# Optimization experiments

Hardware: AMD Instinct MI355X
Metric: run time of the kernel (lower is better)

## Reference

```python
import jax, jax.numpy as jnp
import numpy as np

B = 4
MAX_N = 2048
D = 512
H = 8
HD = D // H
SRC_LENS = [2048, 1536, 1800, 1200]   # sum = 6584
REF_LENS = [1900, 2048, 1400, 1600]   # sum = 6948
NEG_INF = -1e9


def setup_inputs() -> dict:
    key = jax.random.key(0)
    ks = jax.random.split(key, 8)
    n_src, n_ref = sum(SRC_LENS), sum(REF_LENS)
    s = 0.02
    return {
        "feats_src": jax.random.normal(ks[0], (n_src, D), dtype=jnp.float32),
        "batch_src": jnp.asarray(np.repeat(np.arange(B), SRC_LENS), dtype=jnp.int32),
        "feats_ref": jax.random.normal(ks[1], (n_ref, D), dtype=jnp.float32),
        "batch_ref": jnp.asarray(np.repeat(np.arange(B), REF_LENS), dtype=jnp.int32),
        "w_in": jax.random.normal(ks[2], (3 * D, D), dtype=jnp.float32) * s,
        "b_in": jnp.zeros((3 * D,), dtype=jnp.float32),
        "w_out": jax.random.normal(ks[3], (D, D), dtype=jnp.float32) * s,
        "b_out": jnp.zeros((D,), dtype=jnp.float32),
        "gw1": jax.random.normal(ks[4], (D, D), dtype=jnp.float32) * s,
        "gb1": jnp.zeros((D,), dtype=jnp.float32),
        "gw2": jax.random.normal(ks[5], (1, D), dtype=jnp.float32) * s,
        "gb2": jnp.zeros((1,), dtype=jnp.float32),
    }


def _to_dense(feats, batch_idx):
    # sparse [N, D] (sorted batch indices) -> dense [B, MAX_N, D] + key_padding_mask
    n = feats.shape[0]
    counts = jax.ops.segment_sum(jnp.ones((n,), jnp.int32), batch_idx, num_segments=B)
    starts = jnp.concatenate([jnp.zeros((1,), jnp.int32), jnp.cumsum(counts)[:-1].astype(jnp.int32)])
    pos = jnp.arange(n, dtype=jnp.int32) - starts[batch_idx]  # position within batch
    dense = jnp.zeros((B, MAX_N, feats.shape[1]), feats.dtype).at[batch_idx, pos].set(feats)
    mask = jnp.arange(MAX_N)[None, :] >= counts[:, None]  # True = padding (key_padding_mask)
    return dense, mask, pos


def reference(feats_src, batch_src, feats_ref, batch_ref,
              w_in, b_in, w_out, b_out, gw1, gb1, gw2, gb2):
    d_src, mask_src, pos_src = _to_dense(feats_src, batch_src)
    d_ref, mask_ref, _ = _to_dense(feats_ref, batch_ref)

    # nn.MultiheadAttention (batch_first, eval mode): packed in_proj, scaled dot-product
    q = (d_src @ w_in[:D].T + b_in[:D]).reshape(B, MAX_N, H, HD)
    k = (d_ref @ w_in[D:2 * D].T + b_in[D:2 * D]).reshape(B, MAX_N, H, HD)
    v = (d_ref @ w_in[2 * D:].T + b_in[2 * D:]).reshape(B, MAX_N, H, HD)
    scores = jnp.einsum('bqhd,bkhd->bhqk', q * (HD ** -0.5), k)
    scores = jnp.where(mask_ref[:, None, None, :], NEG_INF, scores)
    attn = jax.nn.softmax(scores, axis=-1)
    ctx = jnp.einsum('bhqk,bkhd->bqhd', attn, v).reshape(B, MAX_N, D)
    d_aligned = ctx @ w_out.T + b_out

    # gate MLP: Linear -> ReLU -> Linear -> Sigmoid
    gate = jax.nn.sigmoid(jax.nn.relu(d_aligned @ gw1.T + gb1) @ gw2.T + gb2)  # [B, MAX_N, 1]
    d_out = d_src + gate * d_aligned

    # dense -> ragged: gather each token back to its flat slot
    out_flat = d_out[batch_src, pos_src]  # [N_src, D]
    return out_flat, gate
```

## Files before the change

### kernel.cpp

```cpp
#include <hip/hip_runtime.h>
#include <hip/hip_bf16.h>


typedef __bf16 bf16x8_t __attribute__((ext_vector_type(8)));
typedef __bf16 bf16x4_t __attribute__((ext_vector_type(4)));
typedef float f32x4_t __attribute__((ext_vector_type(4)));
typedef float f32x2_t __attribute__((ext_vector_type(2)));

__device__ inline bf16x8_t zero8() {
  bf16x8_t z;
#pragma unroll
  for (int t = 0; t < 8; ++t) z[t] = (__bf16)0.0f;
  return z;
}

__device__ __forceinline__ int sniff_f32(const void* w) {
  unsigned short u = ((const unsigned short*)w)[threadIdx.x & 63];
  return __ballot((u & 0x7F80) >= 0x3F80) != 0ULL;
}

__global__ void sentinel_k(float* out) {
  if (threadIdx.x == 0 && blockIdx.x == 0) out[0] = 1000.0f;
}

__global__ void cv_all(const void* w_in, const void* b_in, const void* w_out,
                       const void* b_out, const void* gw1, const void* gb1,
                       const void* gw2, const void* gb2,
                       __hip_bfloat16* __restrict__ ws) {
  int f = sniff_f32(w_in);
  const size_t F_W_IN = 16, F_B_IN = 786448, F_W_OUT = 787984, F_B_OUT = 1050128,
               F_GW1 = 1050640, F_GB1 = 1312784, F_GW2 = 1313296, F_GB2 = 1313808;
  const int total = 1313793;
  for (int g = blockIdx.x * 256 + threadIdx.x; g < total; g += gridDim.x * 256) {
    const void* src;
    size_t dst;
    int i;
    if (g < 786432) { src = w_in; dst = F_W_IN; i = g; }
    else if (g < 787968) { src = b_in; dst = F_B_IN; i = g - 786432; }
    else if (g < 1050112) { src = w_out; dst = F_W_OUT; i = g - 787968; }
    else if (g < 1050624) { src = b_out; dst = F_B_OUT; i = g - 1050112; }
    else if (g < 1312768) { src = gw1; dst = F_GW1; i = g - 1050624; }
    else if (g < 1313280) { src = gb1; dst = F_GB1; i = g - 1312768; }
    else if (g < 1313792) { src = gw2; dst = F_GW2; i = g - 1313280; }
    else { src = gb2; dst = F_GB2; i = g - 1313792; }
    ws[dst + i] = f ? __float2bfloat16(((const float*)src)[i])
                    : ((const __hip_bfloat16*)src)[i];
  }
}

template <bool AF32>
__global__ __launch_bounds__(256) void gemm128(
    const void* __restrict__ A_, long aoff, const __hip_bfloat16* __restrict__ Bt,
    const __hip_bfloat16* __restrict__ bias, __hip_bfloat16* __restrict__ C,
    int M, int K, int lda, int ldb, int ldc, float cscale, int relu,
    const void* snf) {
  __shared__ __bf16 As[128][64];
  __shared__ __bf16 Bs[128][64];
  int f = 0;
  if constexpr (AF32) f = sniff_f32(snf);
  int tid = threadIdx.x, lane = tid & 63, wave = tid >> 6;
  int wm = wave >> 1, wn = wave & 1;
  int l15 = lane & 15, quad = lane >> 4;
  int bm = blockIdx.x * 128, bn = blockIdx.y * 128;

  f32x4_t acc[4][4];
#pragma unroll
  for (int i = 0; i < 4; ++i)
#pragma unroll
    for (int j = 0; j < 4; ++j)
#pragma unroll
      for (int r = 0; r < 4; ++r) acc[i][j][r] = 0.f;

  bf16x8_t ra[4], rb[4];
  f32x4_t raf[4][2];

  auto gload = [&](int k0) {
#pragma unroll
    for (int s = 0; s < 4; ++s) {
      int id = s * 256 + tid;
      int row = id >> 3, col = (id & 7) * 8;
      int arow = bm + row;
      if (AF32 && f) {
        if (arow < M) {
          const float* p = (const float*)A_ + aoff + (size_t)arow * lda + k0 + col;
          raf[s][0] = *reinterpret_cast<const f32x4_t*>(p);
          raf[s][1] = *reinterpret_cast<const f32x4_t*>(p + 4);
        } else {
#pragma unroll
          for (int e = 0; e < 4; ++e) { raf[s][0][e] = 0.f; raf[s][1][e] = 0.f; }
        }
      } else {
        ra[s] = (arow < M)
                    ? *reinterpret_cast<const bf16x8_t*>((const __hip_bfloat16*)A_ + aoff +
                                                         (size_t)arow * lda + k0 + col)
                    : zero8();
      }
      rb[s] = *reinterpret_cast<const bf16x8_t*>(Bt + (size_t)(bn + row) * ldb + k0 + col);
    }
  };
  auto stage = [&]() {
#pragma unroll
    for (int s = 0; s < 4; ++s) {
      int id = s * 256 + tid;
      int row = id >> 3, col = (id & 7) * 8;
      if (AF32 && f) {
        bf16x8_t t;
#pragma unroll
        for (int e = 0; e < 4; ++e) {
          t[e] = (__bf16)raf[s][0][e];
          t[4 + e] = (__bf16)raf[s][1][e];
        }
        *reinterpret_cast<bf16x8_t*>(&As[row][col]) = t;
      } else {
        *reinterpret_cast<bf16x8_t*>(&As[row][col]) = ra[s];
      }
      *reinterpret_cast<bf16x8_t*>(&Bs[row][col]) = rb[s];
    }
  };

  int nk = K >> 6;
  gload(0);
  for (int it = 0; it < nk; ++it) {
    stage();
    __syncthreads();
    if (it + 1 < nk) gload((it + 1) * 64);
#pragma unroll
    for (int ks = 0; ks < 2; ++ks) {
      bf16x8_t af[4], bfv[4];
#pragma unroll
      for (int i = 0; i < 4; ++i)
        af[i] = *reinterpret_cast<const bf16x8_t*>(
            &As[wm * 64 + i * 16 + l15][ks * 32 + quad * 8]);
#pragma unroll
      for (int j = 0; j < 4; ++j)
        bfv[j] = *reinterpret_cast<const bf16x8_t*>(
            &Bs[wn * 64 + j * 16 + l15][ks * 32 + quad * 8]);
#pragma unroll
      for (int i = 0; i < 4; ++i)
#pragma unroll
        for (int j = 0; j < 4; ++j)
          acc[i][j] = __builtin_amdgcn_mfma_f32_16x16x32_bf16(af[i], bfv[j], acc[i][j], 0, 0, 0);
    }
    __syncthreads();
  }

#pragma unroll
  for (int i = 0; i < 4; ++i)
#pragma unroll
    for (int j = 0; j < 4; ++j) {
      int col = bn + wn * 64 + j * 16 + l15;
      float bv = __bfloat162float(bias[col]);
#pragma unroll
      for (int r = 0; r < 4; ++r) {
        int row = bm + wm * 64 + i * 16 + quad * 4 + r;
        if (row < M) {
          float v = (acc[i][j][r] + bv) * cscale;
          if (relu) v = fmaxf(v, 0.f);
          C[(size_t)row * ldc + col] = __float2bfloat16(v);
        }
      }
    }
}

__global__ __launch_bounds__(256) void gemm128_pv(
    const __hip_bfloat16* __restrict__ P0, const __hip_bfloat16* __restrict__ P1,
    const float* __restrict__ L, const __hip_bfloat16* __restrict__ Bt,
    const __hip_bfloat16* __restrict__ bias, __hip_bfloat16* __restrict__ C,
    int M) {
  __shared__ __bf16 As[128][64];
  __shared__ __bf16 Bs[128][64];
  int tid = threadIdx.x, lane = tid & 63, wave = tid >> 6;
  int wm = wave >> 1, wn = wave & 1;
  int l15 = lane & 15, quad = lane >> 4;
  int bm = blockIdx.x * 128, bn = blockIdx.y * 128;

  f32x4_t acc[4][4];
#pragma unroll
  for (int i = 0; i < 4; ++i)
#pragma unroll
    for (int j = 0; j < 4; ++j)
#pragma unroll
      for (int r = 0; r < 4; ++r) acc[i][j][r] = 0.f;

  bf16x8_t rp0[4], rp1[4], rb[4];
  f32x2_t rl[4];

  auto gload = [&](int k0) {
    int h = k0 >> 6;
#pragma unroll
    for (int s = 0; s < 4; ++s) {
      int id = s * 256 + tid;
      int row = id >> 3, col = (id & 7) * 8;
      int arow = bm + row;
      if (arow < M) {
        size_t off = (size_t)arow * 512 + k0 + col;
        rp0[s] = *reinterpret_cast<const bf16x8_t*>(P0 + off);
        rp1[s] = *reinterpret_cast<const bf16x8_t*>(P1 + off);
        rl[s] = *reinterpret_cast<const f32x2_t*>(&L[((size_t)arow * 8 + h) * 2]);
      } else {
        rp0[s] = zero8();
        rp1[s] = zero8();
        rl[s][0] = 1.f;
        rl[s][1] = 0.f;
      }
      rb[s] = *reinterpret_cast<const bf16x8_t*>(Bt + (size_t)(bn + row) * 512 + k0 + col);
    }
  };
  auto stage = [&]() {
#pragma unroll
    for (int s = 0; s < 4; ++s) {
      int id = s * 256 + tid;
      int row = id >> 3, col = (id & 7) * 8;
      float sc = 1.0f / (rl[s][0] + rl[s][1]);
      float w0 = rl[s][0] * sc, w1 = rl[s][1] * sc;
      bf16x8_t t;
#pragma unroll
      for (int e = 0; e < 8; ++e)
        t[e] = (__bf16)(w0 * (float)rp0[s][e] + w1 * (float)rp1[s][e]);
      *reinterpret_cast<bf16x8_t*>(&As[row][col]) = t;
      *reinterpret_cast<bf16x8_t*>(&Bs[row][col]) = rb[s];
    }
  };

  gload(0);
  for (int it = 0; it < 8; ++it) {
    stage();
    __syncthreads();
    if (it + 1 < 8) gload((it + 1) * 64);
#pragma unroll
    for (int ks = 0; ks < 2; ++ks) {
      bf16x8_t af[4], bfv[4];
#pragma unroll
      for (int i = 0; i < 4; ++i)
        af[i] = *reinterpret_cast<const bf16x8_t*>(
            &As[wm * 64 + i * 16 + l15][ks * 32 + quad * 8]);
#pragma unroll
      for (int j = 0; j < 4; ++j)
        bfv[j] = *reinterpret_cast<const bf16x8_t*>(
            &Bs[wn * 64 + j * 16 + l15][ks * 32 + quad * 8]);
#pragma unroll
      for (int i = 0; i < 4; ++i)
#pragma unroll
        for (int j = 0; j < 4; ++j)
          acc[i][j] = __builtin_amdgcn_mfma_f32_16x16x32_bf16(af[i], bfv[j], acc[i][j], 0, 0, 0);
    }
    __syncthreads();
  }

#pragma unroll
  for (int i = 0; i < 4; ++i)
#pragma unroll
    for (int j = 0; j < 4; ++j) {
      int col = bn + wn * 64 + j * 16 + l15;
      float bv = __bfloat162float(bias[col]);
#pragma unroll
      for (int r = 0; r < 4; ++r) {
        int row = bm + wm * 64 + i * 16 + quad * 4 + r;
        if (row < M)
          C[(size_t)row * 512 + col] = __float2bfloat16(acc[i][j][r] + bv);
      }
    }
}

__device__ __forceinline__ void flash_core(
    const __hip_bfloat16* __restrict__ Qb, const __hip_bfloat16* __restrict__ KVb,
    __hip_bfloat16* __restrict__ OUTb, float* __restrict__ LPb, int nsrc, int nref,
    int qt, int kt0, int ktNfull, int do_tail,
    __bf16 (&VtL)[2][64][72], __bf16 (&PL)[4][32][72]) {
  int h = blockIdx.y;
  int tid = threadIdx.x, lane = tid & 63, wave = tid >> 6;
  int l15 = lane & 15, quad = lane >> 4;
  int Mb = nsrc + 1;
  int qbase = qt * 128 + wave * 32;

  bf16x8_t qfr[2][2];
#pragma unroll
  for (int g = 0; g < 2; ++g) {
    int qrow = qbase + g * 16 + l15;
#pragma unroll
    for (int ks = 0; ks < 2; ++ks)
      qfr[g][ks] = (qrow < nsrc)
                       ? *reinterpret_cast<const bf16x8_t*>(
                             Qb + (size_t)qrow * 512 + h * 64 + ks * 32 + quad * 8)
                       : zero8();
  }

  f32x4_t O[2][4];
#pragma unroll
  for (int g = 0; g < 2; ++g)
#pragma unroll
    for (int j = 0; j < 4; ++j)
#pragma unroll
      for (int r = 0; r < 4; ++r) O[g][j][r] = 0.f;
  float lsum[2] = {0.f, 0.f};

  bf16x8_t kf[8], v0, v1;
  auto loadK = [&](int k0) {
#pragma unroll
    for (int j = 0; j < 4; ++j) {
      const __hip_bfloat16* kp =
          KVb + (size_t)(k0 + j * 16 + l15) * 1024 + h * 64 + quad * 8;
      kf[j * 2] = *reinterpret_cast<const bf16x8_t*>(kp);
      kf[j * 2 + 1] = *reinterpret_cast<const bf16x8_t*>(kp + 32);
    }
  };
  auto loadV = [&](int k0) {
    const __hip_bfloat16* vp = KVb + (size_t)(k0 + lane) * 1024 + 512 + h * 64 + wave * 16;
    v0 = *reinterpret_cast<const bf16x8_t*>(vp);
    v1 = *reinterpret_cast<const bf16x8_t*>(vp + 8);
  };

  int nit = ktNfull - kt0;
  if (nit > 0) {
    loadK(kt0 * 64);
    loadV(kt0 * 64);
  }

  for (int it = 0; it < nit; ++it) {
    int k0 = (kt0 + it) * 64;
    __bf16(*Vt)[72] = VtL[it & 1];
#pragma unroll
    for (int e = 0; e < 8; ++e) {
      Vt[wave * 16 + e][lane] = v0[e];
      Vt[wave * 16 + 8 + e][lane] = v1[e];
    }
    if (it + 1 < nit) loadV(k0 + 64);

    f32x4_t St[2][4];
#pragma unroll
    for (int g = 0; g < 2; ++g)
#pragma unroll
      for (int j = 0; j < 4; ++j)
#pragma unroll
        for (int r = 0; r < 4; ++r) St[g][j][r] = 0.f;
#pragma unroll
    for (int g = 0; g < 2; ++g)
#pragma unroll
      for (int j = 0; j < 4; ++j)
#pragma unroll
        for (int ks = 0; ks < 2; ++ks)
          St[g][j] = __builtin_amdgcn_mfma_f32_16x16x32_bf16(kf[j * 2 + ks], qfr[g][ks],
                                                             St[g][j], 0, 0, 0);
    if (it + 1 < nit) loadK(k0 + 64);

#pragma unroll
    for (int g = 0; g < 2; ++g)
#pragma unroll
      for (int j = 0; j < 4; ++j) {
        bf16x4_t pk;
#pragma unroll
        for (int r = 0; r < 4; ++r) {
          float p = exp2f(St[g][j][r]);
          lsum[g] += p;
          pk[r] = (__bf16)p;
        }
        *reinterpret_cast<bf16x4_t*>(&PL[wave][g * 16 + l15][j * 16 + quad * 4]) = pk;
      }

    __syncthreads();

    bf16x8_t pa[2][2];
#pragma unroll
    for (int g = 0; g < 2; ++g)
#pragma unroll
      for (int ks = 0; ks < 2; ++ks)
        pa[g][ks] = *reinterpret_cast<const bf16x8_t*>(
            &PL[wave][g * 16 + l15][ks * 32 + quad * 8]);
#pragma unroll
    for (int j = 0; j < 4; ++j)
#pragma unroll
      for (int ks = 0; ks < 2; ++ks) {
        bf16x8_t vb =
            *reinterpret_cast<const bf16x8_t*>(&Vt[j * 16 + l15][ks * 32 + quad * 8]);
#pragma unroll
        for (int g = 0; g < 2; ++g)
          O[g][j] = __builtin_amdgcn_mfma_f32_16x16x32_bf16(pa[g][ks], vb, O[g][j], 0, 0, 0);
      }
  }

  if (do_tail) {
    int k0 = ktNfull * 64;
    __bf16(*Vt)[72] = VtL[nit & 1];
    {
      int kr = k0 + lane;
      const __hip_bfloat16* vp = KVb + (size_t)kr * 1024 + 512 + h * 64 + wave * 16;
      bf16x8_t t0 = (kr < nref) ? *reinterpret_cast<const bf16x8_t*>(vp) : zero8();
      bf16x8_t t1 = (kr < nref) ? *reinterpret_cast<const bf16x8_t*>(vp + 8) : zero8();
#pragma unroll
      for (int e = 0; e < 8; ++e) {
        Vt[wave * 16 + e][lane] = t0[e];
        Vt[wave * 16 + 8 + e][lane] = t1[e];
      }
    }
#pragma unroll
    for (int j = 0; j < 4; ++j) {
      int kcol = k0 + j * 16 + l15;
      const __hip_bfloat16* kp = KVb + (size_t)kcol * 1024 + h * 64 + quad * 8;
      kf[j * 2] = (kcol < nref) ? *reinterpret_cast<const bf16x8_t*>(kp) : zero8();
      kf[j * 2 + 1] = (kcol < nref) ? *reinterpret_cast<const bf16x8_t*>(kp + 32) : zero8();
    }
#pragma unroll
    for (int g = 0; g < 2; ++g) {
      f32x4_t St[4];
#pragma unroll
      for (int j = 0; j < 4; ++j)
#pragma unroll
        for (int r = 0; r < 4; ++r) St[j][r] = 0.f;
#pragma unroll
      for (int j = 0; j < 4; ++j)
#pragma unroll
        for (int ks = 0; ks < 2; ++ks)
          St[j] = __builtin_amdgcn_mfma_f32_16x16x32_bf16(kf[j * 2 + ks], qfr[g][ks],
                                                          St[j], 0, 0, 0);
#pragma unroll
      for (int j = 0; j < 4; ++j) {
        bf16x4_t pk;
#pragma unroll
        for (int r = 0; r < 4; ++r) {
          int kl = k0 + j * 16 + quad * 4 + r;
          float p = (kl < nref) ? exp2f(St[j][r]) : 0.f;
          lsum[g] += p;
          pk[r] = (__bf16)p;
        }
        *reinterpret_cast<bf16x4_t*>(&PL[wave][g * 16 + l15][j * 16 + quad * 4]) = pk;
      }
    }
    __syncthreads();
    bf16x8_t pa[2][2];
#pragma unroll
    for (int g = 0; g < 2; ++g)
#pragma unroll
      for (int ks = 0; ks < 2; ++ks)
        pa[g][ks] = *reinterpret_cast<const bf16x8_t*>(
            &PL[wave][g * 16 + l15][ks * 32 + quad * 8]);
#pragma unroll
    for (int j = 0; j < 4; ++j)
#pragma unroll
      for (int ks = 0; ks < 2; ++ks) {
        bf16x8_t vb =
            *reinterpret_cast<const bf16x8_t*>(&Vt[j * 16 + l15][ks * 32 + quad * 8]);
#pragma unroll
        for (int g = 0; g < 2; ++g)
          O[g][j] = __builtin_amdgcn_mfma_f32_16x16x32_bf16(pa[g][ks], vb, O[g][j], 0, 0, 0);
      }
  }

#pragma unroll
  for (int g = 0; g < 2; ++g) {
    lsum[g] += __shfl_xor(lsum[g], 16);
    lsum[g] += __shfl_xor(lsum[g], 32);
  }

  if (LPb && quad == 0) {
#pragma unroll
    for (int g = 0; g < 2; ++g) {
      int row = qbase + g * 16 + l15;
      if (row < Mb) LPb[((size_t)row * 8 + h) * 2] = lsum[g];
    }
  }

#pragma unroll
  for (int g = 0; g < 2; ++g)
#pragma unroll
    for (int r = 0; r < 4; ++r) {
      int row = qbase + g * 16 + quad * 4 + r;
      if (row < Mb) {
        float li = __shfl(lsum[g], quad * 4 + r);
        float inv = 1.0f / li;
#pragma unroll
        for (int j = 0; j < 4; ++j)
          OUTb[(size_t)row * 512 + h * 64 + j * 16 + l15] =
              __float2bfloat16(O[g][j][r] * inv);
      }
    }
}

__global__ __launch_bounds__(256) void flash_all(
    const __hip_bfloat16* __restrict__ Q, const __hip_bfloat16* __restrict__ KV,
    __hip_bfloat16* __restrict__ O0, __hip_bfloat16* __restrict__ O1,
    float* __restrict__ L, int nsplit) {
  const int TILE_START[4] = {0, 17, 30, 45};
  const int SRC_START[4] = {0, 2048, 3584, 5384};
  const int REF_START[4] = {0, 1900, 3948, 5348};
  const int SRC_LEN[4] = {2048, 1536, 1800, 1200};
  const int REF_LEN[4] = {1900, 2048, 1400, 1600};
  const int CS[4] = {0, 2049, 3586, 5387};
  __shared__ __bf16 VtL[2][64][72];
  __shared__ __bf16 PL[4][32][72];
  int bid = blockIdx.x;
  int b = (bid >= TILE_START[3]) ? 3 : (bid >= TILE_START[2]) ? 2 : (bid >= TILE_START[1]) ? 1 : 0;
  int qt = bid - TILE_START[b];
  int nref = REF_LEN[b];
  int full = nref >> 6, nkt = (nref + 63) >> 6, rem = nref & 63;
  int split = blockIdx.z;
  int kt0, ktN, tail;
  if (nsplit == 1) { kt0 = 0; ktN = full; tail = rem > 0; }
  else if (split == 0) { int half = nkt >> 1; kt0 = 0; ktN = half; tail = 0; }
  else { int half = nkt >> 1; kt0 = half; ktN = full; tail = rem > 0; }
  __hip_bfloat16* OUT = (nsplit == 1 || split == 0) ? O0 : O1;
  float* LP = (nsplit == 1) ? nullptr : (L + split + (size_t)CS[b] * 16);
  flash_core(Q + (size_t)SRC_START[b] * 512, KV + (size_t)REF_START[b] * 1024,
             OUT + (size_t)CS[b] * 512, LP, SRC_LEN[b], nref, qt, kt0, ktN, tail, VtL, PL);
}

__global__ __launch_bounds__(256) void flash_one(const __hip_bfloat16* __restrict__ Qb,
                                                 const __hip_bfloat16* __restrict__ KVb,
                                                 __hip_bfloat16* __restrict__ OUTb,
                                                 int nsrc, int nref) {
  __shared__ __bf16 VtL[2][64][72];
  __shared__ __bf16 PL[4][32][72];
  flash_core(Qb, KVb, OUTb, nullptr, nsrc, nref, blockIdx.x, 0, nref >> 6,
             (nref & 63) > 0, VtL, PL);
}

__global__ __launch_bounds__(256) void finalize_all(
    const void* __restrict__ src, const __hip_bfloat16* __restrict__ aligned,
    const __hip_bfloat16* __restrict__ hidden, const __hip_bfloat16* __restrict__ gw2,
    const __hip_bfloat16* __restrict__ gb2, void* __restrict__ out, const void* snf) {
  int f = sniff_f32(snf);
  int lane = threadIdx.x & 63;
  int r = blockIdx.x * 4 + (threadIdx.x >> 6);
  int b = (r >= 5387) ? 3 : (r >= 3586) ? 2 : (r >= 2049) ? 1 : 0;
  const int CS[4] = {0, 2049, 3586, 5387};
  const int NSRC[4] = {2048, 1536, 1800, 1200};
  int pos = r - CS[b];

  float zacc = 0.f;
  const __hip_bfloat16* hrow = hidden + (size_t)r * 512;
#pragma unroll
  for (int t = 0; t < 8; ++t) {
    int c = lane + (t << 6);
    zacc += __bfloat162float(hrow[c]) * __bfloat162float(gw2[c]);
  }
  for (int o = 32; o; o >>= 1) zacc += __shfl_xor(zacc, o);
  zacc += __bfloat162float(gb2[0]);
  float g = 1.f / (1.f + __expf(-zacc));

  const size_t GOFF = (size_t)6584 * 512;
  if (pos < NSRC[b]) {
    size_t ib = (size_t)(r - b) * 512;
    const __hip_bfloat16* arow = aligned + (size_t)r * 512;
#pragma unroll
    for (int t = 0; t < 8; ++t) {
      int c = lane + (t << 6);
      float sv = f ? ((const float*)src)[ib + c]
                   : __bfloat162float(((const __hip_bfloat16*)src)[ib + c]);
      float val = sv + g * __bfloat162float(arow[c]);
      if (f) ((float*)out)[ib + c] = val;
      else ((__hip_bfloat16*)out)[ib + c] = __float2bfloat16(val);
    }
    if (lane == 0) {
      size_t go = GOFF + b * 2048 + pos;
      if (f) ((float*)out)[go] = g;
      else ((__hip_bfloat16*)out)[go] = __float2bfloat16(g);
    }
  } else {
    for (int p = NSRC[b] + lane; p < 2048; p += 64) {
      size_t go = GOFF + b * 2048 + p;
      if (f) ((float*)out)[go] = g;
      else ((__hip_bfloat16*)out)[go] = __float2bfloat16(g);
    }
  }
}

__global__ __launch_bounds__(256) void finalize_b(
    const void* __restrict__ src, const __hip_bfloat16* __restrict__ alnb,
    const __hip_bfloat16* __restrict__ hidb, const __hip_bfloat16* __restrict__ gw2,
    const __hip_bfloat16* __restrict__ gb2, void* __restrict__ out,
    int b, int nsrc, int src_start, const void* snf) {
  int f = sniff_f32(snf);
  int lane = threadIdx.x & 63;
  int r = blockIdx.x * 4 + (threadIdx.x >> 6);
  if (r > nsrc) return;

  float zacc = 0.f;
  const __hip_bfloat16* hrow = hidb + (size_t)r * 512;
#pragma unroll
  for (int t = 0; t < 8; ++t) {
    int c = lane + (t << 6);
    zacc += __bfloat162float(hrow[c]) * __bfloat162float(gw2[c]);
  }
  for (int o = 32; o; o >>= 1) zacc += __shfl_xor(zacc, o);
  zacc += __bfloat162float(gb2[0]);
  float g = 1.f / (1.f + __expf(-zacc));

  const size_t GOFF = (size_t)6584 * 512;
  if (r < nsrc) {
    size_t ib = (size_t)(src_start + r) * 512;
    const __hip_bfloat16* arow = alnb + (size_t)r * 512;
#pragma unroll
    for (int t = 0; t < 8; ++t) {
      int c = lane + (t << 6);
      float sv = f ? ((const float*)src)[ib + c]
                   : __bfloat162float(((const __hip_bfloat16*)src)[ib + c]);
      float val = sv + g * __bfloat162float(arow[c]);
      if (f) ((float*)out)[ib + c] = val;
      else ((__hip_bfloat16*)out)[ib + c] = __float2bfloat16(val);
    }
    if (lane == 0) {
      size_t go = GOFF + b * 2048 + r;
      if (f) ((float*)out)[go] = g;
      else ((__hip_bfloat16*)out)[go] = __float2bfloat16(g);
    }
  } else {
    for (int p = nsrc + lane; p < 2048; p += 64) {
      size_t go = GOFF + b * 2048 + p;
      if (f) ((float*)out)[go] = g;
      else ((__hip_bfloat16*)out)[go] = __float2bfloat16(g);
    }
  }
}

extern "C" void kernel_launch(void* const* d_in, const int* in_sizes, int n_in,
                              void* d_out, int out_size, void* d_ws, size_t ws_size,
                              hipStream_t stream) {
  (void)in_sizes; (void)n_in; (void)out_size;
  const void* feats_src = d_in[0];
  const void* feats_ref = d_in[2];
  const void* w_in = d_in[4];
  const void* b_in = d_in[5];
  const void* w_out = d_in[6];
  const void* b_out = d_in[7];
  const void* gw1 = d_in[8];
  const void* gb1 = d_in[9];
  const void* gw2 = d_in[10];
  const void* gb2 = d_in[11];

  const size_t F_W_IN = 16, F_B_IN = 786448, F_W_OUT = 787984, F_B_OUT = 1050128,
               F_GW1 = 1050640, F_GB1 = 1312784, F_GW2 = 1313296, F_GB2 = 1313808,
               A0 = 1313824;
  const size_t NEED_A2 = 2 * 22139936;
  const size_t NEED_A = 2 * 15178784;
  const size_t NEED_B = 2 * (A0 + 4259840);
  const float CQ = 0.18033688011112042f;

  if (ws_size < NEED_B) {
    sentinel_k<<<1, 64, 0, stream>>>((float*)d_out);
    return;
  }

  __hip_bfloat16* ws = (__hip_bfloat16*)d_ws;
  cv_all<<<dim3(1024), dim3(256), 0, stream>>>(w_in, b_in, w_out, b_out, gw1, gb1, gw2,
                                               gb2, ws);

  const int SRC_LEN[4] = {2048, 1536, 1800, 1200};
  const int REF_LEN[4] = {1900, 2048, 1400, 1600};
  const int SRC_START[4] = {0, 2048, 3584, 5384};
  const int REF_START[4] = {0, 1900, 3948, 5348};
  dim3 blk(256);

  if (ws_size >= NEED_A) {
    __hip_bfloat16* R1 = ws + A0;
    __hip_bfloat16* R2 = R1 + 3375104;
    __hip_bfloat16* R3 = R2 + 7114752;
    gemm128<true><<<dim3(52, 4), blk, 0, stream>>>(feats_src, 0, ws + F_W_IN,
                                                   ws + F_B_IN, R1, 6584, 512, 512, 512,
                                                   512, CQ, 0, w_in);
    gemm128<true><<<dim3(55, 8), blk, 0, stream>>>(feats_ref, 0, ws + F_W_IN + 262144,
                                                   ws + F_B_IN + 512, R2, 6948, 512, 512,
                                                   512, 1024, 1.0f, 0, w_in);
    if (ws_size >= NEED_A2) {
      __hip_bfloat16* P0 = R3 + 3375104;
      __hip_bfloat16* P1 = P0 + 3375104;
      float* L = (float*)(ws + 21928992);
      flash_all<<<dim3(55, 8, 2), blk, 0, stream>>>(R1, R2, P0, P1, L, 2);
      gemm128_pv<<<dim3(52, 4), blk, 0, stream>>>(P0, P1, L, ws + F_W_OUT, ws + F_B_OUT,
                                                  R1, 6588);
    } else {
      flash_all<<<dim3(55, 8, 1), blk, 0, stream>>>(R1, R2, R3, nullptr, nullptr, 1);
      gemm128<false><<<dim3(52, 4), blk, 0, stream>>>(R3, 0, ws + F_W_OUT, ws + F_B_OUT,
                                                      R1, 6588, 512, 512, 512, 512, 1.0f,
                                                      0, nullptr);
    }
    gemm128<false><<<dim3(52, 4), blk, 0, stream>>>(R1, 0, ws + F_GW1, ws + F_GB1, R3,
                                                    6588, 512, 512, 512, 512, 1.0f, 1,
                                                    nullptr);
    finalize_all<<<dim3(1647), blk, 0, stream>>>(feats_src, R1, R3, ws + F_GW2,
                                                 ws + F_GB2, d_out, w_in);
  } else {
    __hip_bfloat16* W2 = ws + A0;
    __hip_bfloat16* W1 = W2 + 2097152;
    __hip_bfloat16* W3 = W1 + 1081344;
    for (int b = 0; b < 4; ++b) {
      int nsrc = SRC_LEN[b], nref = REF_LEN[b];
      gemm128<true><<<dim3((nsrc + 127) / 128, 4), blk, 0, stream>>>(
          feats_src, (long)SRC_START[b] * 512, ws + F_W_IN, ws + F_B_IN, W1, nsrc, 512,
          512, 512, 512, CQ, 0, w_in);
      gemm128<true><<<dim3((nref + 127) / 128, 8), blk, 0, stream>>>(
          feats_ref, (long)REF_START[b] * 512, ws + F_W_IN + 262144, ws + F_B_IN + 512,
          W2, nref, 512, 512, 512, 1024, 1.0f, 0, w_in);
      flash_one<<<dim3((nsrc + 128) / 128, 8), blk, 0, stream>>>(W1, W2, W3, nsrc, nref);
      gemm128<false><<<dim3((nsrc + 128) / 128, 4), blk, 0, stream>>>(
          W3, 0, ws + F_W_OUT, ws + F_B_OUT, W1, nsrc + 1, 512, 512, 512, 512, 1.0f, 0,
          nullptr);
      gemm128<false><<<dim3((nsrc + 128) / 128, 4), blk, 0, stream>>>(
          W1, 0, ws + F_GW1, ws + F_GB1, W3, nsrc + 1, 512, 512, 512, 512, 1.0f, 1,
          nullptr);
      finalize_b<<<dim3((nsrc + 4) / 4), blk, 0, stream>>>(
          feats_src, W1, W3, ws + F_GW2, ws + F_GB2, d_out, b, nsrc, SRC_START[b], w_in);
    }
  }
}
```

Before: 261.4 us.

## Fuse QKV projections, fold weight conversion into flash, fuse gate MLP with finalize

Merges the Q and KV projection GEMMs into one launch that reads fp32 inputs and weights directly, converting them while staging into shared memory. This drops the w_in conversion pass. The remaining weight conversion moves into extra blocks of the flash attention grid, so it overlaps with attention work. The gate MLP (GEMM, ReLU, dot with gw2, sigmoid) is fused with the residual finalize, so the hidden activation is never written out. In exchange, the fused gate kernel runs on only 103 blocks and recomputes its B tiles, which may underuse the GPU.

```diff
diff --git a/kernel.cpp b/kernel.cpp
--- a/kernel.cpp
+++ b/kernel.cpp
@@ -6,6 +6,8 @@
 typedef __bf16 bf16x4_t __attribute__((ext_vector_type(4)));
 typedef float f32x4_t __attribute__((ext_vector_type(4)));
 typedef float f32x2_t __attribute__((ext_vector_type(2)));
+
+#define CQ_SCALE 0.18033688011112042f
 
 __device__ inline bf16x8_t zero8() {
   bf16x8_t z;
@@ -48,6 +50,138 @@
   }
 }
 
+__device__ __forceinline__ void proj_core(
+    const void* __restrict__ A_, const void* __restrict__ B_,
+    const void* __restrict__ bias_, long biasoff, __hip_bfloat16* __restrict__ C,
+    int M, int ldc, float cscale, int f, int brow0, int bm, int bn,
+    __bf16 (&As)[128][64], __bf16 (&Bs)[128][64]) {
+  int tid = threadIdx.x, lane = tid & 63, wave = tid >> 6;
+  int wm = wave >> 1, wn = wave & 1;
+  int l15 = lane & 15, quad = lane >> 4;
+
+  f32x4_t acc[4][4];
+#pragma unroll
+  for (int i = 0; i < 4; ++i)
+#pragma unroll
+    for (int j = 0; j < 4; ++j)
+#pragma unroll
+      for (int r = 0; r < 4; ++r) acc[i][j][r] = 0.f;
+
+  bf16x8_t ra[4], rb[4];
+  f32x4_t raf[4][2], rbf[4][2];
+
+  auto gload = [&](int k0) {
+#pragma unroll
+    for (int s = 0; s < 4; ++s) {
+      int id = s * 256 + tid;
+      int row = id >> 3, col = (id & 7) * 8;
+      int arow = bm + row;
+      size_t boffe = (size_t)(brow0 + bn + row) * 512 + k0 + col;
+      if (f) {
+        if (arow < M) {
+          const float* p = (const float*)A_ + (size_t)arow * 512 + k0 + col;
+          raf[s][0] = *reinterpret_cast<const f32x4_t*>(p);
+          raf[s][1] = *reinterpret_cast<const f32x4_t*>(p + 4);
+        } else {
+#pragma unroll
+          for (int e = 0; e < 4; ++e) { raf[s][0][e] = 0.f; raf[s][1][e] = 0.f; }
+        }
+        const float* q = (const float*)B_ + boffe;
+        rbf[s][0] = *reinterpret_cast<const f32x4_t*>(q);
+        rbf[s][1] = *reinterpret_cast<const f32x4_t*>(q + 4);
+      } else {
+        ra[s] = (arow < M)
+                    ? *reinterpret_cast<const bf16x8_t*>((const __hip_bfloat16*)A_ +
+                                                         (size_t)arow * 512 + k0 + col)
+                    : zero8();
+        rb[s] = *reinterpret_cast<const bf16x8_t*>((const __hip_bfloat16*)B_ + boffe);
+      }
+    }
+  };
+  auto stage = [&]() {
+#pragma unroll
+    for (int s = 0; s < 4; ++s) {
+      int id = s * 256 + tid;
+      int row = id >> 3, col = (id & 7) * 8;
+      if (f) {
+        bf16x8_t ta, tb;
+#pragma unroll
+        for (int e = 0; e < 4; ++e) {
+          ta[e] = (__bf16)raf[s][0][e];
+          ta[4 + e] = (__bf16)raf[s][1][e];
+          tb[e] = (__bf16)rbf[s][0][e];
+          tb[4 + e] = (__bf16)rbf[s][1][e];
+        }
+        *reinterpret_cast<bf16x8_t*>(&As[row][col]) = ta;
+        *reinterpret_cast<bf16x8_t*>(&Bs[row][col]) = tb;
+      } else {
+        *reinterpret_cast<bf16x8_t*>(&As[row][col]) = ra[s];
+        *reinterpret_cast<bf16x8_t*>(&Bs[row][col]) = rb[s];
+      }
+    }
+  };
+
+  gload(0);
+  for (int it = 0; it < 8; ++it) {
+    stage();
+    __syncthreads();
+    if (it + 1 < 8) gload((it + 1) * 64);
+#pragma unroll
+    for (int ks = 0; ks < 2; ++ks) {
+      bf16x8_t af[4], bfv[4];
+#pragma unroll
+      for (int i = 0; i < 4; ++i)
+        af[i] = *reinterpret_cast<const bf16x8_t*>(
+            &As[wm * 64 + i * 16 + l15][ks * 32 + quad * 8]);
+#pragma unroll
+      for (int j = 0; j < 4; ++j)
+        bfv[j] = *reinterpret_cast<const bf16x8_t*>(
+            &Bs[wn * 64 + j * 16 + l15][ks * 32 + quad * 8]);
+#pragma unroll
+      for (int i = 0; i < 4; ++i)
+#pragma unroll
+        for (int j = 0; j < 4; ++j)
+          acc[i][j] = __builtin_amdgcn_mfma_f32_16x16x32_bf16(af[i], bfv[j], acc[i][j], 0, 0, 0);
+    }
+    __syncthreads();
+  }
+
+#pragma unroll
+  for (int i = 0; i < 4; ++i)
+#pragma unroll
+    for (int j = 0; j < 4; ++j) {
+      int col = bn + wn * 64 + j * 16 + l15;
+      float bv = f ? ((const float*)bias_)[biasoff + col]
+                   : __bfloat162float(((const __hip_bfloat16*)bias_)[biasoff + col]);
+#pragma unroll
+      for (int r = 0; r < 4; ++r) {
+        int row = bm + wm * 64 + i * 16 + quad * 4 + r;
+        if (row < M)
+          C[(size_t)row * ldc + col] = __float2bfloat16((acc[i][j][r] + bv) * cscale);
+      }
+    }
+}
+
+__global__ __launch_bounds__(256) void proj_all(
+    const void* __restrict__ fs, const void* __restrict__ fr,
+    const void* __restrict__ w_in_, const void* __restrict__ b_in_,
+    __hip_bfloat16* __restrict__ Q, __hip_bfloat16* __restrict__ KV) {
+  __shared__ __bf16 As[128][64];
+  __shared__ __bf16 Bs[128][64];
+  int f = sniff_f32(w_in_);
+  int bid = blockIdx.x;
+  if (bid < 208) {
+    int bx = bid >> 2, by = bid & 3;
+    proj_core(fs, w_in_, b_in_, 0, Q, 6584, 512, CQ_SCALE, f, 0, bx * 128, by * 128,
+              As, Bs);
+  } else {
+    int k = bid - 208;
+    int bx = k >> 3, by = k & 7;
+    proj_core(fr, w_in_, b_in_, 512, KV, 6948, 1024, 1.0f, f, 512, bx * 128, by * 128,
+              As, Bs);
+  }
+}
+
 template <bool AF32>
 __global__ __launch_bounds__(256) void gemm128(
     const void* __restrict__ A_, long aoff, const __hip_bfloat16* __restrict__ Bt,
@@ -370,11 +504,11 @@
     for (int j = 0; j < 4; ++j)
 #pragma unroll
       for (int ks = 0; ks < 2; ++ks) {
-        bf16x8_t vb =
+        bf16x8_t vbf =
             *reinterpret_cast<const bf16x8_t*>(&Vt[j * 16 + l15][ks * 32 + quad * 8]);
 #pragma unroll
         for (int g = 0; g < 2; ++g)
-          O[g][j] = __builtin_amdgcn_mfma_f32_16x16x32_bf16(pa[g][ks], vb, O[g][j], 0, 0, 0);
+          O[g][j] = __builtin_amdgcn_mfma_f32_16x16x32_bf16(pa[g][ks], vbf, O[g][j], 0, 0, 0);
       }
   }
 
@@ -437,11 +571,11 @@
     for (int j = 0; j < 4; ++j)
 #pragma unroll
       for (int ks = 0; ks < 2; ++ks) {
-        bf16x8_t vb =
+        bf16x8_t vbf =
             *reinterpret_cast<const bf16x8_t*>(&Vt[j * 16 + l15][ks * 32 + quad * 8]);
 #pragma unroll
         for (int g = 0; g < 2; ++g)
-          O[g][j] = __builtin_amdgcn_mfma_f32_16x16x32_bf16(pa[g][ks], vb, O[g][j], 0, 0, 0);
+          O[g][j] = __builtin_amdgcn_mfma_f32_16x16x32_bf16(pa[g][ks], vbf, O[g][j], 0, 0, 0);
       }
   }
 
@@ -478,15 +612,38 @@
 __global__ __launch_bounds__(256) void flash_all(
     const __hip_bfloat16* __restrict__ Q, const __hip_bfloat16* __restrict__ KV,
     __hip_bfloat16* __restrict__ O0, __hip_bfloat16* __restrict__ O1,
-    float* __restrict__ L, int nsplit) {
+    float* __restrict__ L, int nsplit, const void* w_out, const void* b_out,
+    const void* gw1, const void* gb1, const void* gw2, const void* gb2,
+    __hip_bfloat16* __restrict__ ws, const void* snf) {
+  __shared__ __bf16 VtL[2][64][72];
+  __shared__ __bf16 PL[4][32][72];
+  if (blockIdx.x >= 55) {
+    int f = sniff_f32(snf);
+    int nconv = 2 * gridDim.y * gridDim.z;
+    int cid = ((blockIdx.x - 55) * gridDim.y + blockIdx.y) * gridDim.z + blockIdx.z;
+    const size_t F_W_OUT = 787984, F_B_OUT = 1050128, F_GW1 = 1050640,
+                 F_GB1 = 1312784, F_GW2 = 1313296, F_GB2 = 1313808;
+    for (int g = cid * 256 + threadIdx.x; g < 525825; g += nconv * 256) {
+      const void* src;
+      size_t dst;
+      int i;
+      if (g < 262144) { src = w_out; dst = F_W_OUT; i = g; }
+      else if (g < 262656) { src = b_out; dst = F_B_OUT; i = g - 262144; }
+      else if (g < 524800) { src = gw1; dst = F_GW1; i = g - 262656; }
+      else if (g < 525312) { src = gb1; dst = F_GB1; i = g - 524800; }
+      else if (g < 525824) { src = gw2; dst = F_GW2; i = g - 525312; }
+      else { src = gb2; dst = F_GB2; i = g - 525824; }
+      ws[dst + i] = f ? __float2bfloat16(((const float*)src)[i])
+                      : ((const __hip_bfloat16*)src)[i];
+    }
+    return;
+  }
   const int TILE_START[4] = {0, 17, 30, 45};
   const int SRC_START[4] = {0, 2048, 3584, 5384};
   const int REF_START[4] = {0, 1900, 3948, 5348};
   const int SRC_LEN[4] = {2048, 1536, 1800, 1200};
   const int REF_LEN[4] = {1900, 2048, 1400, 1600};
   const int CS[4] = {0, 2049, 3586, 5387};
-  __shared__ __bf16 VtL[2][64][72];
-  __shared__ __bf16 PL[4][32][72];
   int bid = blockIdx.x;
   int b = (bid >= TILE_START[3]) ? 3 : (bid >= TILE_START[2]) ? 2 : (bid >= TILE_START[1]) ? 1 : 0;
   int qt = bid - TILE_START[b];
@@ -513,52 +670,133 @@
              (nref & 63) > 0, VtL, PL);
 }
 
-__global__ __launch_bounds__(256) void finalize_all(
-    const void* __restrict__ src, const __hip_bfloat16* __restrict__ aligned,
-    const __hip_bfloat16* __restrict__ hidden, const __hip_bfloat16* __restrict__ gw2,
-    const __hip_bfloat16* __restrict__ gb2, void* __restrict__ out, const void* snf) {
-  int f = sniff_f32(snf);
-  int lane = threadIdx.x & 63;
-  int r = blockIdx.x * 4 + (threadIdx.x >> 6);
-  int b = (r >= 5387) ? 3 : (r >= 3586) ? 2 : (r >= 2049) ? 1 : 0;
+__global__ __launch_bounds__(256) void gate_fin(
+    const void* __restrict__ src, const __hip_bfloat16* __restrict__ ALN,
+    const __hip_bfloat16* __restrict__ gw1b, const __hip_bfloat16* __restrict__ gb1b,
+    const __hip_bfloat16* __restrict__ gw2b, const __hip_bfloat16* __restrict__ gb2b,
+    void* __restrict__ out, const void* snf) {
+  __shared__ __bf16 As[64][64];
+  __shared__ __bf16 Bs[128][64];
   const int CS[4] = {0, 2049, 3586, 5387};
   const int NSRC[4] = {2048, 1536, 1800, 1200};
-  int pos = r - CS[b];
-
-  float zacc = 0.f;
-  const __hip_bfloat16* hrow = hidden + (size_t)r * 512;
-#pragma unroll
-  for (int t = 0; t < 8; ++t) {
-    int c = lane + (t << 6);
-    zacc += __bfloat162float(hrow[c]) * __bfloat162float(gw2[c]);
-  }
-  for (int o = 32; o; o >>= 1) zacc += __shfl_xor(zacc, o);
-  zacc += __bfloat162float(gb2[0]);
-  float g = 1.f / (1.f + __expf(-zacc));
+  int f = sniff_f32(snf);
+  int tid = threadIdx.x, lane = tid & 63, w = tid >> 6;
+  int l15 = lane & 15, quad = lane >> 4;
+  int bm = blockIdx.x * 64;
+
+  float gacc[4] = {0.f, 0.f, 0.f, 0.f};
+  bf16x8_t ra[2], rb[4];
+
+  for (int ct = 0; ct < 4; ++ct) {
+    int bnn = ct * 128;
+    f32x4_t acc[8];
+#pragma unroll
+    for (int j = 0; j < 8; ++j)
+#pragma unroll
+      for (int r = 0; r < 4; ++r) acc[j][r] = 0.f;
+
+    auto gload = [&](int k0) {
+#pragma unroll
+      for (int s = 0; s < 2; ++s) {
+        int id = s * 256 + tid;
+        int row = id >> 3, col = (id & 7) * 8;
+        int arow = bm + row;
+        ra[s] = (arow < 6588)
+                    ? *reinterpret_cast<const bf16x8_t*>(ALN + (size_t)arow * 512 + k0 + col)
+                    : zero8();
+      }
+#pragma unroll
+      for (int s = 0; s < 4; ++s) {
+        int id = s * 256 + tid;
+        int row = id >> 3, col = (id & 7) * 8;
+        rb[s] = *reinterpret_cast<const bf16x8_t*>(gw1b + (size_t)(bnn + row) * 512 + k0 + col);
+      }
+    };
+    auto stage = [&]() {
+#pragma unroll
+      for (int s = 0; s < 2; ++s) {
+        int id = s * 256 + tid;
+        *reinterpret_cast<bf16x8_t*>(&As[id >> 3][(id & 7) * 8]) = ra[s];
+      }
+#pragma unroll
+      for (int s = 0; s < 4; ++s) {
+        int id = s * 256 + tid;
+        *reinterpret_cast<bf16x8_t*>(&Bs[id >> 3][(id & 7) * 8]) = rb[s];
+      }
+    };
+
+    gload(0);
+    for (int it = 0; it < 8; ++it) {
+      stage();
+      __syncthreads();
+      if (it + 1 < 8) gload((it + 1) * 64);
+#pragma unroll
+      for (int ks = 0; ks < 2; ++ks) {
+        bf16x8_t af = *reinterpret_cast<const bf16x8_t*>(
+            &As[w * 16 + l15][ks * 32 + quad * 8]);
+#pragma unroll
+        for (int j = 0; j < 8; ++j) {
+          bf16x8_t bv = *reinterpret_cast<const bf16x8_t*>(
+              &Bs[j * 16 + l15][ks * 32 + quad * 8]);
+          acc[j] = __builtin_amdgcn_mfma_f32_16x16x32_bf16(af, bv, acc[j], 0, 0, 0);
+        }
+      }
+      __syncthreads();
+    }
+
+#pragma unroll
+    for (int j = 0; j < 8; ++j) {
+      int col = bnn + j * 16 + l15;
+      float b1 = __bfloat162float(gb1b[col]);
+      float w2 = __bfloat162float(gw2b[col]);
+#pragma unroll
+      for (int r = 0; r < 4; ++r) gacc[r] += fmaxf(acc[j][r] + b1, 0.f) * w2;
+    }
+  }
+
+#pragma unroll
+  for (int r = 0; r < 4; ++r) {
+    gacc[r] += __shfl_xor(gacc[r], 1);
+    gacc[r] += __shfl_xor(gacc[r], 2);
+    gacc[r] += __shfl_xor(gacc[r], 4);
+    gacc[r] += __shfl_xor(gacc[r], 8);
+  }
+  float gb2v = __bfloat162float(gb2b[0]);
+  float gv[4];
+#pragma unroll
+  for (int r = 0; r < 4; ++r) gv[r] = 1.f / (1.f + __expf(-(gacc[r] + gb2v)));
 
   const size_t GOFF = (size_t)6584 * 512;
-  if (pos < NSRC[b]) {
-    size_t ib = (size_t)(r - b) * 512;
-    const __hip_bfloat16* arow = aligned + (size_t)r * 512;
-#pragma unroll
-    for (int t = 0; t < 8; ++t) {
-      int c = lane + (t << 6);
-      float sv = f ? ((const float*)src)[ib + c]
-                   : __bfloat162float(((const __hip_bfloat16*)src)[ib + c]);
-      float val = sv + g * __bfloat162float(arow[c]);
-      if (f) ((float*)out)[ib + c] = val;
-      else ((__hip_bfloat16*)out)[ib + c] = __float2bfloat16(val);
-    }
-    if (lane == 0) {
-      size_t go = GOFF + b * 2048 + pos;
-      if (f) ((float*)out)[go] = g;
-      else ((__hip_bfloat16*)out)[go] = __float2bfloat16(g);
-    }
-  } else {
-    for (int p = NSRC[b] + lane; p < 2048; p += 64) {
-      size_t go = GOFF + b * 2048 + p;
-      if (f) ((float*)out)[go] = g;
-      else ((__hip_bfloat16*)out)[go] = __float2bfloat16(g);
+#pragma unroll
+  for (int rr = 0; rr < 16; ++rr) {
+    int row = bm + w * 16 + rr;
+    if (row >= 6588) continue;
+    float g = __shfl(gv[rr & 3], (rr >> 2) * 16);
+    int b = (row >= 5387) ? 3 : (row >= 3586) ? 2 : (row >= 2049) ? 1 : 0;
+    int pos = row - CS[b];
+    if (pos < NSRC[b]) {
+      size_t ib = (size_t)(row - b) * 512;
+      const __hip_bfloat16* arow = ALN + (size_t)row * 512;
+#pragma unroll
+      for (int t = 0; t < 8; ++t) {
+        int c = lane + (t << 6);
+        float sv = f ? ((const float*)src)[ib + c]
+                     : __bfloat162float(((const __hip_bfloat16*)src)[ib + c]);
+        float val = sv + g * __bfloat162float(arow[c]);
+        if (f) ((float*)out)[ib + c] = val;
+        else ((__hip_bfloat16*)out)[ib + c] = __float2bfloat16(val);
+      }
+      if (lane == 0) {
+        size_t go = GOFF + b * 2048 + pos;
+        if (f) ((float*)out)[go] = g;
+        else ((__hip_bfloat16*)out)[go] = __float2bfloat16(g);
+      }
+    } else {
+      for (int p = NSRC[b] + lane; p < 2048; p += 64) {
+        size_t go = GOFF + b * 2048 + p;
+        if (f) ((float*)out)[go] = g;
+        else ((__hip_bfloat16*)out)[go] = __float2bfloat16(g);
+      }
     }
   }
 }
@@ -632,7 +870,6 @@
   const size_t NEED_A2 = 2 * 22139936;
   const size_t NEED_A = 2 * 15178784;
   const size_t NEED_B = 2 * (A0 + 4259840);
-  const float CQ = 0.18033688011112042f;
 
   if (ws_size < NEED_B) {
     sentinel_k<<<1, 64, 0, stream>>>((float*)d_out);
@@ -640,9 +877,6 @@
   }
 
   __hip_bfloat16* ws = (__hip_bfloat16*)d_ws;
-  cv_all<<<dim3(1024), dim3(256), 0, stream>>>(w_in, b_in, w_out, b_out, gw1, gb1, gw2,
-                                               gb2, ws);
-
   const int SRC_LEN[4] = {2048, 1536, 1800, 1200};
   const int REF_LEN[4] = {1900, 2048, 1400, 1600};
   const int SRC_START[4] = {0, 2048, 3584, 5384};
@@ -653,31 +887,28 @@
     __hip_bfloat16* R1 = ws + A0;
     __hip_bfloat16* R2 = R1 + 3375104;
     __hip_bfloat16* R3 = R2 + 7114752;
-    gemm128<true><<<dim3(52, 4), blk, 0, stream>>>(feats_src, 0, ws + F_W_IN,
-                                                   ws + F_B_IN, R1, 6584, 512, 512, 512,
-                                                   512, CQ, 0, w_in);
-    gemm128<true><<<dim3(55, 8), blk, 0, stream>>>(feats_ref, 0, ws + F_W_IN + 262144,
-                                                   ws + F_B_IN + 512, R2, 6948, 512, 512,
-                                                   512, 1024, 1.0f, 0, w_in);
+    proj_all<<<dim3(648), blk, 0, stream>>>(feats_src, feats_ref, w_in, b_in, R1, R2);
     if (ws_size >= NEED_A2) {
       __hip_bfloat16* P0 = R3 + 3375104;
       __hip_bfloat16* P1 = P0 + 3375104;
       float* L = (float*)(ws + 21928992);
-      flash_all<<<dim3(55, 8, 2), blk, 0, stream>>>(R1, R2, P0, P1, L, 2);
+      flash_all<<<dim3(57, 8, 2), blk, 0, stream>>>(R1, R2, P0, P1, L, 2, w_out, b_out,
+                                                    gw1, gb1, gw2, gb2, ws, w_in);
       gemm128_pv<<<dim3(52, 4), blk, 0, stream>>>(P0, P1, L, ws + F_W_OUT, ws + F_B_OUT,
                                                   R1, 6588);
     } else {
-      flash_all<<<dim3(55, 8, 1), blk, 0, stream>>>(R1, R2, R3, nullptr, nullptr, 1);
+      flash_all<<<dim3(57, 8, 1), blk, 0, stream>>>(R1, R2, R3, nullptr, nullptr, 1,
+                                                    w_out, b_out, gw1, gb1, gw2, gb2, ws,
+                                                    w_in);
       gemm128<false><<<dim3(52, 4), blk, 0, stream>>>(R3, 0, ws + F_W_OUT, ws + F_B_OUT,
                                                       R1, 6588, 512, 512, 512, 512, 1.0f,
                                                       0, nullptr);
     }
-    gemm128<false><<<dim3(52, 4), blk, 0, stream>>>(R1, 0, ws + F_GW1, ws + F_GB1, R3,
-                                                    6588, 512, 512, 512, 512, 1.0f, 1,
-                                                    nullptr);
-    finalize_all<<<dim3(1647), blk, 0, stream>>>(feats_src, R1, R3, ws + F_GW2,
-                                                 ws + F_GB2, d_out, w_in);
+    gate_fin<<<dim3(103), blk, 0, stream>>>(feats_src, R1, ws + F_GW1, ws + F_GB1,
+                                            ws + F_GW2, ws + F_GB2, d_out, w_in);
   } else {
+    cv_all<<<dim3(1024), blk, 0, stream>>>(w_in, b_in, w_out, b_out, gw1, gb1, gw2, gb2,
+                                           ws);
     __hip_bfloat16* W2 = ws + A0;
     __hip_bfloat16* W1 = W2 + 2097152;
     __hip_bfloat16* W3 = W1 + 1081344;
@@ -685,7 +916,7 @@
       int nsrc = SRC_LEN[b], nref = REF_LEN[b];
       gemm128<true><<<dim3((nsrc + 127) / 128, 4), blk, 0, stream>>>(
           feats_src, (long)SRC_START[b] * 512, ws + F_W_IN, ws + F_B_IN, W1, nsrc, 512,
-          512, 512, 512, CQ, 0, w_in);
+          512, 512, 512, CQ_SCALE, 0, w_in);
       gemm128<true><<<dim3((nref + 127) / 128, 8), blk, 0, stream>>>(
           feats_ref, (long)REF_START[b] * 512, ws + F_W_IN + 262144, ws + F_B_IN + 512,
           W2, nref, 512, 512, 512, 1024, 1.0f, 0, w_in);
```

After: 346.7 us. 1.33x slower.
